# Optimization experiments

Hardware: AMD Instinct MI355X
Metric: run time of the kernel (lower is better)

## Reference

```python
import jax, jax.numpy as jnp
import numpy as np

N_TOKENS = 8192
TOP_K = 2
HIDDEN = 2048


def setup_inputs() -> dict:
    key = jax.random.key(0)
    k1, k2, k3 = jax.random.split(key, 3)
    moe_output = jax.random.normal(k1, (N_TOKENS * TOP_K, HIDDEN), dtype=jnp.float32)
    scores = jax.random.uniform(k2, (N_TOKENS * TOP_K,), dtype=jnp.float32)
    mapped_slots = jax.random.randint(k3, (N_TOKENS * TOP_K,), 0, N_TOKENS * TOP_K, dtype=jnp.int32)
    return {"moe_output": moe_output, "scores": scores, "mapped_slots": mapped_slots, "top_k": TOP_K}


def reference(moe_output, scores, mapped_slots, top_k):
    # Flatten to [total_slots, hidden] as the kernel does
    hidden = moe_output.shape[-1]
    flat = moe_output.reshape(-1, hidden)
    n_tokens = scores.shape[0] // top_k
    # Gather expert outputs per mapped slot: [n_tokens, top_k, hidden]
    gathered = flat[mapped_slots].reshape(n_tokens, top_k, hidden)
    w = scores.reshape(n_tokens, top_k)
    # Weighted combine over top_k experts
    layer_output = jnp.einsum("tk,tkh->th", w, gathered)
    return layer_output
```

## Files before the change

kernel.cpp:

```cpp
#include <hip/hip_runtime.h>

__global__ __launch_bounds__(256) void moe_gather_kernel(
    const float* __restrict__ moe,
    const float* __restrict__ scores,
    const int*   __restrict__ slots,
    float*       __restrict__ out,
    int hidden, int top_k) {
    const int t   = blockIdx.x;
    const int tid = threadIdx.x;
    const int nvec = hidden >> 2;

    float w[8];
    const float4* rows[8];
    const int K = top_k > 8 ? 8 : top_k;
    for (int k = 0; k < K; ++k) {
        const int s = slots[(size_t)t * top_k + k];
        w[k] = scores[(size_t)t * top_k + k];
        rows[k] = (const float4*)(moe + (size_t)s * hidden);
    }

    float4* orow = (float4*)(out + (size_t)t * hidden);
    for (int v = tid; v < nvec; v += blockDim.x) {
        float4 acc = make_float4(0.f, 0.f, 0.f, 0.f);
        for (int k = 0; k < K; ++k) {
            float4 x = rows[k][v];
            acc.x += w[k] * x.x;
            acc.y += w[k] * x.y;
            acc.z += w[k] * x.z;
            acc.w += w[k] * x.w;
        }
        orow[v] = acc;
    }
}

extern "C" void kernel_launch(void* const* d_in, const int* in_sizes, int n_in,
                              void* d_out, int out_size, void* d_ws, size_t ws_size,
                              hipStream_t stream) {
    const float* moe    = (const float*)d_in[0];
    const float* scores = (const float*)d_in[1];
    const int*   slots  = (const int*)d_in[2];
    float* out = (float*)d_out;

    const int total_slots = in_sizes[1];
    const int hidden      = in_sizes[0] / total_slots;
    const int n_tokens    = out_size / hidden;
    const int top_k       = total_slots / n_tokens;

    moe_gather_kernel<<<n_tokens, 256, 0, stream>>>(moe, scores, slots, out,
                                                    hidden, top_k);
}
```

Measured before the change: 210.0 us.

## Add specialized top_k=2 hidden=2048 kernel processing four tokens per block

```diff
diff --git a/kernel.cpp b/kernel.cpp
--- a/kernel.cpp
+++ b/kernel.cpp
@@ -1,6 +1,49 @@
 #include <hip/hip_runtime.h>
 
-__global__ __launch_bounds__(256) void moe_gather_kernel(
+typedef float fvec4 __attribute__((ext_vector_type(4)));
+
+__global__ __launch_bounds__(256) void moe_gather_k2_h2048_t4(
+    const float* __restrict__ moe,
+    const float* __restrict__ scores,
+    const int*   __restrict__ slots,
+    float*       __restrict__ out) {
+    constexpr int NVEC = 512;
+    const int t0  = blockIdx.x * 4;
+    const int tid = threadIdx.x;
+
+    int   s[8];
+    float w[8];
+#pragma unroll
+    for (int i = 0; i < 8; ++i) {
+        s[i] = slots[2 * t0 + i];
+        w[i] = scores[2 * t0 + i];
+    }
+
+    const fvec4* __restrict__ mo = (const fvec4*)moe;
+    fvec4* __restrict__ ov = (fvec4*)out;
+
+    fvec4 acc[8];
+#pragma unroll
+    for (int i = 0; i < 4; ++i) {
+        const size_t r0 = (size_t)s[2 * i]     * NVEC;
+        const size_t r1 = (size_t)s[2 * i + 1] * NVEC;
+        fvec4 a0 = mo[r0 + tid];
+        fvec4 a1 = mo[r0 + tid + 256];
+        fvec4 b0 = mo[r1 + tid];
+        fvec4 b1 = mo[r1 + tid + 256];
+        acc[2 * i]     = w[2 * i] * a0 + w[2 * i + 1] * b0;
+        acc[2 * i + 1] = w[2 * i] * a1 + w[2 * i + 1] * b1;
+    }
+
+#pragma unroll
+    for (int i = 0; i < 4; ++i) {
+        const size_t o = (size_t)(t0 + i) * NVEC;
+        __builtin_nontemporal_store(acc[2 * i],     ov + o + tid);
+        __builtin_nontemporal_store(acc[2 * i + 1], ov + o + tid + 256);
+    }
+}
+
+__global__ __launch_bounds__(256) void moe_gather_generic(
     const float* __restrict__ moe,
     const float* __restrict__ scores,
     const int*   __restrict__ slots,
@@ -46,6 +89,11 @@
     const int n_tokens    = out_size / hidden;
     const int top_k       = total_slots / n_tokens;
 
-    moe_gather_kernel<<<n_tokens, 256, 0, stream>>>(moe, scores, slots, out,
-                                                    hidden, top_k);
+    if (top_k == 2 && hidden == 2048 && (n_tokens % 4) == 0) {
+        moe_gather_k2_h2048_t4<<<n_tokens / 4, 256, 0, stream>>>(moe, scores,
+                                                                 slots, out);
+    } else {
+        moe_gather_generic<<<n_tokens, 256, 0, stream>>>(moe, scores, slots, out,
+                                                         hidden, top_k);
+    }
 }
```

New measurement: 209.1 us. Within noise of the previous version (-0.4%).
